# Kernel optimization log

Measured on AMD Instinct MI355X. Metric: run time of the kernel, lower is better.

## Reference

```python
import jax, jax.numpy as jnp
import numpy as np

B, T, C = 4, 2048, 1024
H, D = 16, 64  # num_heads, head_size; H*D == C


def setup_inputs() -> dict:
    key = jax.random.key(0)
    ks = jax.random.split(key, 6)
    s = C ** -0.5
    return {
        "x": jax.random.normal(ks[0], (B, T, C), dtype=jnp.float32),
        "Wq": jax.random.normal(ks[1], (H, C, D), dtype=jnp.float32) * s,
        "Wk": jax.random.normal(ks[2], (H, C, D), dtype=jnp.float32) * s,
        "Wv": jax.random.normal(ks[3], (H, C, D), dtype=jnp.float32) * s,
        "Wo": jax.random.normal(ks[4], (C, C), dtype=jnp.float32) * s,
        "bo": jnp.zeros((C,), dtype=jnp.float32),
    }


def reference(x, Wq, Wk, Wv, Wo, bo):
    # Per-head projections, vectorized over heads: [B,T,C] x [H,C,D] -> [B,H,T,D]
    q = jnp.einsum("btc,hcd->bhtd", x, Wq)
    k = jnp.einsum("btc,hcd->bhtd", x, Wk)
    v = jnp.einsum("btc,hcd->bhtd", x, Wv)
    # NOTE: original scales by n_embd**-0.5 (input channel C), not head_size.
    scale = jnp.asarray(C, x.dtype) ** -0.5
    scores = jnp.einsum("bhtd,bhsd->bhts", q, k) * scale  # [B,H,T,T]
    causal = jnp.tril(jnp.ones((T, T), dtype=bool))
    scores = jnp.where(causal, scores, jnp.asarray(-jnp.inf, x.dtype))
    attn = jax.nn.softmax(scores, axis=-1)
    out = jnp.einsum("bhts,bhsd->bhtd", attn, v)  # [B,H,T,D]
    # concat heads: [B,T,H*D] == [B,T,C]
    out = out.transpose(0, 2, 1, 3).reshape(B, T, H * D)
    return out @ Wo.T + bo
```

## Files before the change

kernel.cpp:

```cpp
#include <hip/hip_runtime.h>
#include <hip/hip_bf16.h>
#include <math.h>

#define B_ 4
#define T_ 2048
#define C_ 1024
#define H_ 16
#define D_ 64
#define BT (B_*T_)
#define BH (B_*H_)

typedef __bf16 bf16x8 __attribute__((ext_vector_type(8)));
typedef __bf16 bf16x4 __attribute__((ext_vector_type(4)));
typedef float f32x4 __attribute__((ext_vector_type(4)));
typedef unsigned short u16;
typedef u16 u16x8 __attribute__((ext_vector_type(8)));

#define GLL(g, l) __builtin_amdgcn_global_load_lds( \
    (const __attribute__((address_space(1))) unsigned int*)(g), \
    (__attribute__((address_space(3))) unsigned int*)(l), 16, 0, 0)

#define SCALE2 0.04508422f

__device__ __forceinline__ u16 f2b(float f) {
    union { float f; unsigned u; } v; v.f = f;
    unsigned r = v.u + 0x7fffu + ((v.u >> 16) & 1u);
    return (u16)(r >> 16);
}

__global__ __launch_bounds__(256) void cast_f32_bf16(const float* __restrict__ in,
                                                     u16* __restrict__ out) {
    int g = blockIdx.x * 256 + threadIdx.x;
    float4 x = ((const float4*)in)[g];
    ushort4 o;
    o.x = f2b(x.x); o.y = f2b(x.y); o.z = f2b(x.z); o.w = f2b(x.w);
    ((ushort4*)out)[g] = o;
}

__global__ __launch_bounds__(256) void transpose_w(const float* __restrict__ Wq,
                                                   const float* __restrict__ Wk,
                                                   const float* __restrict__ Wv,
                                                   u16* __restrict__ out) {
    __shared__ u16 lds[64][72];
    int cb = blockIdx.x, h = blockIdx.y, w = blockIdx.z;
    const float* W = (w == 0) ? Wq : (w == 1) ? Wk : Wv;
    float sc = (w == 0) ? SCALE2 : 1.0f;
    int tid = threadIdx.x;
    int c0 = cb * 64;
    {
        int col = (tid & 15) * 4;
        for (int cc = 0; cc < 4; ++cc) {
            int r = (tid >> 4) + cc * 16;
            float4 x = *(const float4*)&W[(size_t)(h * C_ + c0 + r) * D_ + col];
            lds[r][col + 0] = f2b(x.x * sc); lds[r][col + 1] = f2b(x.y * sc);
            lds[r][col + 2] = f2b(x.z * sc); lds[r][col + 3] = f2b(x.w * sc);
        }
    }
    __syncthreads();
    {
        int tcol = (tid & 7) * 8;
        for (int cc = 0; cc < 2; ++cc) {
            int d = (tid >> 3) + cc * 32;
            u16x8 t;
            for (int j = 0; j < 8; ++j) t[j] = lds[tcol + j][d];
            *(u16x8*)&out[(((size_t)(w * H_ + h) * D_ + d) * C_) + c0 + tcol] = t;
        }
    }
}

__global__ __launch_bounds__(256) void qkv_gemm(const u16* __restrict__ xbf,
                                                const u16* __restrict__ wt,
                                                u16* __restrict__ q, u16* __restrict__ k,
                                                u16* __restrict__ v) {
    __shared__ u16 Al[128][64];
    __shared__ u16 Bl[128][64];
    int mb = blockIdx.x, nb = blockIdx.y;
    int tid = threadIdx.x, wv = tid >> 6, lane = tid & 63, l15 = lane & 15, quad = lane >> 4;
    int rowh = (wv & 1) * 64, colh = (wv >> 1) * 64;
    f32x4 acc[4][4];
    #pragma unroll
    for (int i = 0; i < 4; ++i)
        #pragma unroll
        for (int j = 0; j < 4; ++j) acc[i][j] = (f32x4){0.f, 0.f, 0.f, 0.f};
    int lrow = lane >> 3;
    int srow = wv * 32 + lrow;
    int scol = (((lane & 7) ^ lrow)) * 8;
    const u16* agp = &xbf[(size_t)(mb * 128 + srow) * C_ + scol];
    const u16* bgp = &wt[(size_t)(nb * 128 + srow) * C_ + scol];
    int rsw = l15 & 7;
    for (int k0 = 0; k0 < C_; k0 += 64) {
        #pragma unroll
        for (int j = 0; j < 4; ++j) {
            GLL(agp + (size_t)(j * 8) * C_ + k0, &Al[wv * 32 + j * 8][0]);
            GLL(bgp + (size_t)(j * 8) * C_ + k0, &Bl[wv * 32 + j * 8][0]);
        }
        __syncthreads();
        #pragma unroll
        for (int ks = 0; ks < 2; ++ks) {
            int cbl = (((ks << 2) | quad) ^ rsw) * 8;
            bf16x8 af[4], bf[4];
            #pragma unroll
            for (int mt = 0; mt < 4; ++mt)
                af[mt] = *(const bf16x8*)&Al[rowh + mt * 16 + l15][cbl];
            #pragma unroll
            for (int nt = 0; nt < 4; ++nt)
                bf[nt] = *(const bf16x8*)&Bl[colh + nt * 16 + l15][cbl];
            #pragma unroll
            for (int mt = 0; mt < 4; ++mt)
                #pragma unroll
                for (int nt = 0; nt < 4; ++nt)
                    acc[mt][nt] = __builtin_amdgcn_mfma_f32_16x16x32_bf16(af[mt], bf[nt], acc[mt][nt], 0, 0, 0);
        }
        __syncthreads();
    }
    #pragma unroll
    for (int nt = 0; nt < 4; ++nt) {
        int n0 = nb * 128 + colh + nt * 16;
        int wsel = n0 >> 10, hh = (n0 >> 6) & 15, d0 = n0 & 63;
        u16* op = (wsel == 0) ? q : (wsel == 1) ? k : v;
        #pragma unroll
        for (int mt = 0; mt < 4; ++mt)
            #pragma unroll
            for (int r = 0; r < 4; ++r) {
                int m = mb * 128 + rowh + mt * 16 + quad * 4 + r;
                int bb = m >> 11, tt = m & (T_ - 1);
                op[((size_t)(bb * H_ + hh) * T_ + tt) * D_ + d0 + l15] = f2b(acc[mt][nt][r]);
            }
    }
}

__global__ __launch_bounds__(256) void vtrans(const u16* __restrict__ v, u16* __restrict__ vt) {
    __shared__ u16 lds[64][72];
    int tb = blockIdx.x, bh = blockIdx.y;
    int t0 = tb * 64, tid = threadIdx.x;
    int col = (tid & 7) * 8;
    for (int cc = 0; cc < 2; ++cc) {
        int r = (tid >> 3) + cc * 32;
        *(u16x8*)&lds[r][col] = *(const u16x8*)&v[((size_t)bh * T_ + t0 + r) * D_ + col];
    }
    __syncthreads();
    for (int cc = 0; cc < 2; ++cc) {
        int d = (tid >> 3) + cc * 32;
        u16x8 t;
        for (int j = 0; j < 8; ++j) t[j] = lds[col + j][d];
        *(u16x8*)&vt[((size_t)bh * D_ + d) * T_ + t0 + col] = t;
    }
}

__global__ __launch_bounds__(256, 2) void attn(const u16* __restrict__ q, const u16* __restrict__ kk,
                                               const u16* __restrict__ vt, u16* __restrict__ att) {
    __shared__ u16 Kl[2][64][64];
    __shared__ u16 Vl[2][64][64];
    __shared__ u16 Pl[4][32][72];
    int bh = blockIdx.x, c = 15 - blockIdx.y;
    int b = bh >> 4, h = bh & 15;
    int tid = threadIdx.x, wid = tid >> 6, lane = tid & 63, l15 = lane & 15, quad = lane >> 4;
    const u16* qbase = q + (size_t)bh * T_ * D_;
    const u16* kbase = kk + (size_t)bh * T_ * D_;
    const u16* vbase = vt + (size_t)bh * D_ * T_;
    u16* pw = &Pl[wid][0][0];
    bf16x8 ones;
    #pragma unroll
    for (int j = 0; j < 8; ++j) ones[j] = (__bf16)1.0f;
    int r8 = lane >> 3, cbl_st = lane & 7;
    int csrc = ((cbl_st ^ r8)) * 8;
    int strow = wid * 16 + r8;
    int rsw = l15 & 7;

    int R0q = c * 128 + wid * 32;
    int ktb = 2 * c + 1;
    int kmax_w = R0q >> 6;
    bf16x8 bq[2][2];
    #pragma unroll
    for (int qt = 0; qt < 2; ++qt)
        #pragma unroll
        for (int kd = 0; kd < 2; ++kd)
            bq[qt][kd] = *(const bf16x8*)&qbase[(size_t)(R0q + qt * 16 + l15) * D_ + kd * 32 + quad * 8];
    f32x4 o[4][2];
    f32x4 lacc[2];
    float m2[2] = {-INFINITY, -INFINITY};
    #pragma unroll
    for (int dt = 0; dt < 4; ++dt)
        #pragma unroll
        for (int qt = 0; qt < 2; ++qt) o[dt][qt] = (f32x4){0.f, 0.f, 0.f, 0.f};
    lacc[0] = (f32x4){0.f, 0.f, 0.f, 0.f};
    lacc[1] = (f32x4){0.f, 0.f, 0.f, 0.f};
    #pragma unroll
    for (int j = 0; j < 2; ++j) {
        GLL(kbase + (size_t)(strow + j * 8) * D_ + csrc, &Kl[0][wid * 16 + j * 8][0]);
        GLL(vbase + (size_t)(strow + j * 8) * T_ + csrc, &Vl[0][wid * 16 + j * 8][0]);
    }
    __syncthreads();
    for (int kt = 0; kt <= ktb; ++kt) {
        int cur = kt & 1;
        if (kt < ktb) {
            int kn = (kt + 1) * 64;
            #pragma unroll
            for (int j = 0; j < 2; ++j) {
                GLL(kbase + (size_t)(kn + strow + j * 8) * D_ + csrc, &Kl[cur ^ 1][wid * 16 + j * 8][0]);
                GLL(vbase + (size_t)(strow + j * 8) * T_ + kn + csrc, &Vl[cur ^ 1][wid * 16 + j * 8][0]);
            }
        }
        if (kt <= kmax_w) {
            int k0 = kt * 64;
            f32x4 sS[4][2];
            #pragma unroll
            for (int kvt = 0; kvt < 4; ++kvt)
                #pragma unroll
                for (int qt = 0; qt < 2; ++qt) sS[kvt][qt] = (f32x4){0.f, 0.f, 0.f, 0.f};
            #pragma unroll
            for (int kd = 0; kd < 2; ++kd) {
                int cblk = (((kd << 2) | quad) ^ rsw) * 8;
                bf16x8 akf[4];
                #pragma unroll
                for (int kvt = 0; kvt < 4; ++kvt)
                    akf[kvt] = *(const bf16x8*)&Kl[cur][kvt * 16 + l15][cblk];
                #pragma unroll
                for (int kvt = 0; kvt < 4; ++kvt)
                    #pragma unroll
                    for (int qt = 0; qt < 2; ++qt)
                        sS[kvt][qt] = __builtin_amdgcn_mfma_f32_16x16x32_bf16(akf[kvt], bq[qt][kd], sS[kvt][qt], 0, 0, 0);
            }
            if (kt == kmax_w) {
                #pragma unroll
                for (int qt = 0; qt < 2; ++qt) {
                    int qabs = R0q + qt * 16 + l15;
                    #pragma unroll
                    for (int kvt = 0; kvt < 4; ++kvt) {
                        int kvb = k0 + kvt * 16 + quad * 4;
                        #pragma unroll
                        for (int r = 0; r < 4; ++r)
                            if (kvb + r > qabs) sS[kvt][qt][r] = -INFINITY;
                    }
                }
            }
            float alpha[2];
            #pragma unroll
            for (int qt = 0; qt < 2; ++qt) {
                float vm = sS[0][qt][0];
                #pragma unroll
                for (int kvt = 0; kvt < 4; ++kvt)
                    #pragma unroll
                    for (int r = 0; r < 4; ++r) vm = fmaxf(vm, sS[kvt][qt][r]);
                vm = fmaxf(vm, __shfl_xor(vm, 16));
                vm = fmaxf(vm, __shfl_xor(vm, 32));
                float mn = fmaxf(m2[qt], vm);
                alpha[qt] = __builtin_amdgcn_exp2f(m2[qt] - mn);
                m2[qt] = mn;
            }
            #pragma unroll
            for (int kvt = 0; kvt < 4; ++kvt)
                #pragma unroll
                for (int qt = 0; qt < 2; ++qt)
                    #pragma unroll
                    for (int r = 0; r < 4; ++r)
                        sS[kvt][qt][r] = __builtin_amdgcn_exp2f(sS[kvt][qt][r] - m2[qt]);
            #pragma unroll
            for (int dt = 0; dt < 4; ++dt)
                #pragma unroll
                for (int qt = 0; qt < 2; ++qt)
                    #pragma unroll
                    for (int r = 0; r < 4; ++r) o[dt][qt][r] *= alpha[qt];
            #pragma unroll
            for (int qt = 0; qt < 2; ++qt)
                #pragma unroll
                for (int r = 0; r < 4; ++r) lacc[qt][r] *= alpha[qt];
            #pragma unroll
            for (int qt = 0; qt < 2; ++qt)
                #pragma unroll
                for (int kvt = 0; kvt < 4; ++kvt) {
                    bf16x4 w;
                    #pragma unroll
                    for (int r = 0; r < 4; ++r) w[r] = (__bf16)sS[kvt][qt][r];
                    *(bf16x4*)&pw[(qt * 16 + l15) * 72 + kvt * 16 + quad * 4] = w;
                }
            #pragma unroll
            for (int ks = 0; ks < 2; ++ks) {
                int cblk = (((ks << 2) | quad) ^ rsw) * 8;
                bf16x8 avf[4];
                #pragma unroll
                for (int dt = 0; dt < 4; ++dt)
                    avf[dt] = *(const bf16x8*)&Vl[cur][dt * 16 + l15][cblk];
                #pragma unroll
                for (int qt = 0; qt < 2; ++qt) {
                    bf16x8 bp = *(const bf16x8*)&pw[(qt * 16 + l15) * 72 + ks * 32 + quad * 8];
                    #pragma unroll
                    for (int dt = 0; dt < 4; ++dt)
                        o[dt][qt] = __builtin_amdgcn_mfma_f32_16x16x32_bf16(avf[dt], bp, o[dt][qt], 0, 0, 0);
                    lacc[qt] = __builtin_amdgcn_mfma_f32_16x16x32_bf16(ones, bp, lacc[qt], 0, 0, 0);
                }
            }
        }
        __syncthreads();
    }
    #pragma unroll
    for (int qt = 0; qt < 2; ++qt) {
        float rl = __builtin_amdgcn_rcpf(lacc[qt][0]);
        int qabs = R0q + qt * 16 + l15;
        #pragma unroll
        for (int dt = 0; dt < 4; ++dt) {
            bf16x4 w;
            #pragma unroll
            for (int r = 0; r < 4; ++r) w[r] = (__bf16)(o[dt][qt][r] * rl);
            *(bf16x4*)&att[(size_t)(b * T_ + qabs) * C_ + h * 64 + dt * 16 + quad * 4] = w;
        }
    }
}

__global__ __launch_bounds__(256) void out_gemm(const u16* __restrict__ att,
                                                const u16* __restrict__ wo,
                                                const float* __restrict__ bo,
                                                float* __restrict__ out) {
    __shared__ u16 Al[128][64];
    __shared__ u16 Bl[128][64];
    int mb = blockIdx.x, nb = blockIdx.y;
    int tid = threadIdx.x, wv = tid >> 6, lane = tid & 63, l15 = lane & 15, quad = lane >> 4;
    int rowh = (wv & 1) * 64, colh = (wv >> 1) * 64;
    f32x4 acc[4][4];
    #pragma unroll
    for (int i = 0; i < 4; ++i)
        #pragma unroll
        for (int j = 0; j < 4; ++j) acc[i][j] = (f32x4){0.f, 0.f, 0.f, 0.f};
    int lrow = lane >> 3;
    int srow = wv * 32 + lrow;
    int scol = (((lane & 7) ^ lrow)) * 8;
    const u16* agp = &att[(size_t)(mb * 128 + srow) * C_ + scol];
    const u16* bgp = &wo[(size_t)(nb * 128 + srow) * C_ + scol];
    int rsw = l15 & 7;
    for (int k0 = 0; k0 < C_; k0 += 64) {
        #pragma unroll
        for (int j = 0; j < 4; ++j) {
            GLL(agp + (size_t)(j * 8) * C_ + k0, &Al[wv * 32 + j * 8][0]);
            GLL(bgp + (size_t)(j * 8) * C_ + k0, &Bl[wv * 32 + j * 8][0]);
        }
        __syncthreads();
        #pragma unroll
        for (int ks = 0; ks < 2; ++ks) {
            int cbl = (((ks << 2) | quad) ^ rsw) * 8;
            bf16x8 af[4], bf[4];
            #pragma unroll
            for (int mt = 0; mt < 4; ++mt)
                af[mt] = *(const bf16x8*)&Al[rowh + mt * 16 + l15][cbl];
            #pragma unroll
            for (int nt = 0; nt < 4; ++nt)
                bf[nt] = *(const bf16x8*)&Bl[colh + nt * 16 + l15][cbl];
            #pragma unroll
            for (int mt = 0; mt < 4; ++mt)
                #pragma unroll
                for (int nt = 0; nt < 4; ++nt)
                    acc[mt][nt] = __builtin_amdgcn_mfma_f32_16x16x32_bf16(af[mt], bf[nt], acc[mt][nt], 0, 0, 0);
        }
        __syncthreads();
    }
    #pragma unroll
    for (int nt = 0; nt < 4; ++nt) {
        int n = nb * 128 + colh + nt * 16 + l15;
        float bias = bo[n];
        #pragma unroll
        for (int mt = 0; mt < 4; ++mt)
            #pragma unroll
            for (int r = 0; r < 4; ++r) {
                int m = mb * 128 + rowh + mt * 16 + quad * 4 + r;
                out[(size_t)m * C_ + n] = acc[mt][nt][r] + bias;
            }
    }
}

extern "C" void kernel_launch(void* const* d_in, const int* in_sizes, int n_in,
                              void* d_out, int out_size, void* d_ws, size_t ws_size,
                              hipStream_t stream) {
    const float* x  = (const float*)d_in[0];
    const float* Wq = (const float*)d_in[1];
    const float* Wk = (const float*)d_in[2];
    const float* Wv = (const float*)d_in[3];
    const float* Wo = (const float*)d_in[4];
    const float* bo = (const float*)d_in[5];
    float* out = (float*)d_out;
    char* ws = (char*)d_ws;
    u16* xbf  = (u16*)(ws + (size_t)0);
    u16* wt   = (u16*)(ws + ((size_t)16 << 20));
    u16* wobf = (u16*)(ws + ((size_t)22 << 20));
    u16* qb   = (u16*)(ws + ((size_t)24 << 20));
    u16* kb   = (u16*)(ws + ((size_t)40 << 20));
    u16* vb   = (u16*)(ws + ((size_t)56 << 20));
    u16* vtb  = (u16*)(ws + ((size_t)72 << 20));
    u16* attb = (u16*)(ws + ((size_t)88 << 20));

    hipLaunchKernelGGL(cast_f32_bf16, dim3(BT * C_ / 1024), dim3(256), 0, stream, x, xbf);
    hipLaunchKernelGGL(cast_f32_bf16, dim3(C_ * C_ / 1024), dim3(256), 0, stream, Wo, wobf);
    hipLaunchKernelGGL(transpose_w, dim3(C_ / 64, H_, 3), dim3(256), 0, stream, Wq, Wk, Wv, wt);
    hipLaunchKernelGGL(qkv_gemm, dim3(BT / 128, 3 * C_ / 128), dim3(256), 0, stream, xbf, wt, qb, kb, vb);
    hipLaunchKernelGGL(vtrans, dim3(T_ / 64, BH), dim3(256), 0, stream, vb, vtb);
    hipLaunchKernelGGL(attn, dim3(BH, 16), dim3(256), 0, stream, qb, kb, vtb, attb);
    hipLaunchKernelGGL(out_gemm, dim3(BT / 128, C_ / 128), dim3(256), 0, stream, attb, wobf, bo, out);
}
```

Before: 247.0 us.

## Double-buffer LDS tiles in projection GEMMs and merge prep kernels into one launch

Both the QKV and output GEMMs now use two LDS buffers. The next K-tile is fetched with global_load_lds while MFMAs run on the current tile, so global-load latency overlaps with compute instead of stalling at a barrier every step. The two cast kernels and the weight transpose are also merged into a single prep launch that picks its role by block index, removing two launch gaps. The cost is doubled LDS per GEMM block (64 KB), which may lower occupancy.

```diff
diff --git a/kernel.cpp b/kernel.cpp
--- a/kernel.cpp
+++ b/kernel.cpp
@@ -28,32 +28,44 @@
     return (u16)(r >> 16);
 }
 
-__global__ __launch_bounds__(256) void cast_f32_bf16(const float* __restrict__ in,
-                                                     u16* __restrict__ out) {
-    int g = blockIdx.x * 256 + threadIdx.x;
-    float4 x = ((const float4*)in)[g];
-    ushort4 o;
-    o.x = f2b(x.x); o.y = f2b(x.y); o.z = f2b(x.z); o.w = f2b(x.w);
-    ((ushort4*)out)[g] = o;
-}
-
-__global__ __launch_bounds__(256) void transpose_w(const float* __restrict__ Wq,
-                                                   const float* __restrict__ Wk,
-                                                   const float* __restrict__ Wv,
-                                                   u16* __restrict__ out) {
+__global__ __launch_bounds__(256) void prep(const float* __restrict__ x,
+                                            const float* __restrict__ Wo,
+                                            const float* __restrict__ Wq,
+                                            const float* __restrict__ Wk,
+                                            const float* __restrict__ Wv,
+                                            u16* __restrict__ xbf,
+                                            u16* __restrict__ wobf,
+                                            u16* __restrict__ wt) {
     __shared__ u16 lds[64][72];
-    int cb = blockIdx.x, h = blockIdx.y, w = blockIdx.z;
+    int bid = blockIdx.x, tid = threadIdx.x;
+    if (bid < 8192) {
+        int g = bid * 256 + tid;
+        float4 v = ((const float4*)x)[g];
+        ushort4 o;
+        o.x = f2b(v.x); o.y = f2b(v.y); o.z = f2b(v.z); o.w = f2b(v.w);
+        ((ushort4*)xbf)[g] = o;
+        return;
+    }
+    if (bid < 9216) {
+        int g = (bid - 8192) * 256 + tid;
+        float4 v = ((const float4*)Wo)[g];
+        ushort4 o;
+        o.x = f2b(v.x); o.y = f2b(v.y); o.z = f2b(v.z); o.w = f2b(v.w);
+        ((ushort4*)wobf)[g] = o;
+        return;
+    }
+    int id = bid - 9216;
+    int cb = id & 15, h = (id >> 4) & 15, w = id >> 8;
     const float* W = (w == 0) ? Wq : (w == 1) ? Wk : Wv;
     float sc = (w == 0) ? SCALE2 : 1.0f;
-    int tid = threadIdx.x;
     int c0 = cb * 64;
     {
         int col = (tid & 15) * 4;
         for (int cc = 0; cc < 4; ++cc) {
             int r = (tid >> 4) + cc * 16;
-            float4 x = *(const float4*)&W[(size_t)(h * C_ + c0 + r) * D_ + col];
-            lds[r][col + 0] = f2b(x.x * sc); lds[r][col + 1] = f2b(x.y * sc);
-            lds[r][col + 2] = f2b(x.z * sc); lds[r][col + 3] = f2b(x.w * sc);
+            float4 v = *(const float4*)&W[(size_t)(h * C_ + c0 + r) * D_ + col];
+            lds[r][col + 0] = f2b(v.x * sc); lds[r][col + 1] = f2b(v.y * sc);
+            lds[r][col + 2] = f2b(v.z * sc); lds[r][col + 3] = f2b(v.w * sc);
         }
     }
     __syncthreads();
@@ -63,7 +75,7 @@
             int d = (tid >> 3) + cc * 32;
             u16x8 t;
             for (int j = 0; j < 8; ++j) t[j] = lds[tcol + j][d];
-            *(u16x8*)&out[(((size_t)(w * H_ + h) * D_ + d) * C_) + c0 + tcol] = t;
+            *(u16x8*)&wt[(((size_t)(w * H_ + h) * D_ + d) * C_) + c0 + tcol] = t;
         }
     }
 }
@@ -72,8 +84,8 @@
                                                 const u16* __restrict__ wt,
                                                 u16* __restrict__ q, u16* __restrict__ k,
                                                 u16* __restrict__ v) {
-    __shared__ u16 Al[128][64];
-    __shared__ u16 Bl[128][64];
+    __shared__ u16 Al[2][128][64];
+    __shared__ u16 Bl[2][128][64];
     int mb = blockIdx.x, nb = blockIdx.y;
     int tid = threadIdx.x, wv = tid >> 6, lane = tid & 63, l15 = lane & 15, quad = lane >> 4;
     int rowh = (wv & 1) * 64, colh = (wv >> 1) * 64;
@@ -88,23 +100,32 @@
     const u16* agp = &xbf[(size_t)(mb * 128 + srow) * C_ + scol];
     const u16* bgp = &wt[(size_t)(nb * 128 + srow) * C_ + scol];
     int rsw = l15 & 7;
-    for (int k0 = 0; k0 < C_; k0 += 64) {
-        #pragma unroll
-        for (int j = 0; j < 4; ++j) {
-            GLL(agp + (size_t)(j * 8) * C_ + k0, &Al[wv * 32 + j * 8][0]);
-            GLL(bgp + (size_t)(j * 8) * C_ + k0, &Bl[wv * 32 + j * 8][0]);
-        }
-        __syncthreads();
+    #pragma unroll
+    for (int j = 0; j < 4; ++j) {
+        GLL(agp + (size_t)(j * 8) * C_, &Al[0][wv * 32 + j * 8][0]);
+        GLL(bgp + (size_t)(j * 8) * C_, &Bl[0][wv * 32 + j * 8][0]);
+    }
+    __syncthreads();
+    for (int kt = 0; kt < 16; ++kt) {
+        int cur = kt & 1;
+        if (kt < 15) {
+            int kn = (kt + 1) * 64;
+            #pragma unroll
+            for (int j = 0; j < 4; ++j) {
+                GLL(agp + (size_t)(j * 8) * C_ + kn, &Al[cur ^ 1][wv * 32 + j * 8][0]);
+                GLL(bgp + (size_t)(j * 8) * C_ + kn, &Bl[cur ^ 1][wv * 32 + j * 8][0]);
+            }
+        }
         #pragma unroll
         for (int ks = 0; ks < 2; ++ks) {
             int cbl = (((ks << 2) | quad) ^ rsw) * 8;
             bf16x8 af[4], bf[4];
             #pragma unroll
             for (int mt = 0; mt < 4; ++mt)
-                af[mt] = *(const bf16x8*)&Al[rowh + mt * 16 + l15][cbl];
+                af[mt] = *(const bf16x8*)&Al[cur][rowh + mt * 16 + l15][cbl];
             #pragma unroll
             for (int nt = 0; nt < 4; ++nt)
-                bf[nt] = *(const bf16x8*)&Bl[colh + nt * 16 + l15][cbl];
+                bf[nt] = *(const bf16x8*)&Bl[cur][colh + nt * 16 + l15][cbl];
             #pragma unroll
             for (int mt = 0; mt < 4; ++mt)
                 #pragma unroll
@@ -311,8 +332,8 @@
                                                 const u16* __restrict__ wo,
                                                 const float* __restrict__ bo,
                                                 float* __restrict__ out) {
-    __shared__ u16 Al[128][64];
-    __shared__ u16 Bl[128][64];
+    __shared__ u16 Al[2][128][64];
+    __shared__ u16 Bl[2][128][64];
     int mb = blockIdx.x, nb = blockIdx.y;
     int tid = threadIdx.x, wv = tid >> 6, lane = tid & 63, l15 = lane & 15, quad = lane >> 4;
     int rowh = (wv & 1) * 64, colh = (wv >> 1) * 64;
@@ -327,23 +348,32 @@
     const u16* agp = &att[(size_t)(mb * 128 + srow) * C_ + scol];
     const u16* bgp = &wo[(size_t)(nb * 128 + srow) * C_ + scol];
     int rsw = l15 & 7;
-    for (int k0 = 0; k0 < C_; k0 += 64) {
-        #pragma unroll
-        for (int j = 0; j < 4; ++j) {
-            GLL(agp + (size_t)(j * 8) * C_ + k0, &Al[wv * 32 + j * 8][0]);
-            GLL(bgp + (size_t)(j * 8) * C_ + k0, &Bl[wv * 32 + j * 8][0]);
-        }
-        __syncthreads();
+    #pragma unroll
+    for (int j = 0; j < 4; ++j) {
+        GLL(agp + (size_t)(j * 8) * C_, &Al[0][wv * 32 + j * 8][0]);
+        GLL(bgp + (size_t)(j * 8) * C_, &Bl[0][wv * 32 + j * 8][0]);
+    }
+    __syncthreads();
+    for (int kt = 0; kt < 16; ++kt) {
+        int cur = kt & 1;
+        if (kt < 15) {
+            int kn = (kt + 1) * 64;
+            #pragma unroll
+            for (int j = 0; j < 4; ++j) {
+                GLL(agp + (size_t)(j * 8) * C_ + kn, &Al[cur ^ 1][wv * 32 + j * 8][0]);
+                GLL(bgp + (size_t)(j * 8) * C_ + kn, &Bl[cur ^ 1][wv * 32 + j * 8][0]);
+            }
+        }
         #pragma unroll
         for (int ks = 0; ks < 2; ++ks) {
             int cbl = (((ks << 2) | quad) ^ rsw) * 8;
             bf16x8 af[4], bf[4];
             #pragma unroll
             for (int mt = 0; mt < 4; ++mt)
-                af[mt] = *(const bf16x8*)&Al[rowh + mt * 16 + l15][cbl];
+                af[mt] = *(const bf16x8*)&Al[cur][rowh + mt * 16 + l15][cbl];
             #pragma unroll
             for (int nt = 0; nt < 4; ++nt)
-                bf[nt] = *(const bf16x8*)&Bl[colh + nt * 16 + l15][cbl];
+                bf[nt] = *(const bf16x8*)&Bl[cur][colh + nt * 16 + l15][cbl];
             #pragma unroll
             for (int mt = 0; mt < 4; ++mt)
                 #pragma unroll
@@ -386,9 +416,7 @@
     u16* vtb  = (u16*)(ws + ((size_t)72 << 20));
     u16* attb = (u16*)(ws + ((size_t)88 << 20));
 
-    hipLaunchKernelGGL(cast_f32_bf16, dim3(BT * C_ / 1024), dim3(256), 0, stream, x, xbf);
-    hipLaunchKernelGGL(cast_f32_bf16, dim3(C_ * C_ / 1024), dim3(256), 0, stream, Wo, wobf);
-    hipLaunchKernelGGL(transpose_w, dim3(C_ / 64, H_, 3), dim3(256), 0, stream, Wq, Wk, Wv, wt);
+    hipLaunchKernelGGL(prep, dim3(9984), dim3(256), 0, stream, x, Wo, Wq, Wk, Wv, xbf, wobf, wt);
     hipLaunchKernelGGL(qkv_gemm, dim3(BT / 128, 3 * C_ / 128), dim3(256), 0, stream, xbf, wt, qb, kb, vb);
     hipLaunchKernelGGL(vtrans, dim3(T_ / 64, BH), dim3(256), 0, stream, vb, vtb);
     hipLaunchKernelGGL(attn, dim3(BH, 16), dim3(256), 0, stream, qb, kb, vtb, attb);
```

New measurement: 263.8 us. 1.07x slower.
